# Optimization experiments

Hardware: AMD Instinct MI355X
Metric: run time of the kernel (lower is better)

## Reference

```python
import jax, jax.numpy as jnp
import numpy as np

BN_EPS = 1e-5
L2_EPS = 1e-12

def _conv2d(x, w, pad):
    # x: NCHW, w: OIHW
    return jax.lax.conv_general_dilated(
        x, w, window_strides=(1, 1), padding=[(pad, pad), (pad, pad)],
        dimension_numbers=('NCHW', 'OIHW', 'NCHW'))

def _l2norm(x, axis):
    n = jnp.sqrt(jnp.sum(x * x, axis=axis, keepdims=True))
    return x / jnp.maximum(n, L2_EPS)

def setup_inputs() -> dict:
    key = jax.random.key(0)
    ks = jax.random.split(key, 8)
    x = jax.random.normal(ks[0], (16, 512, 32, 32), dtype=jnp.float32)
    w_proj1 = jax.random.normal(ks[1], (512, 512, 3, 3), dtype=jnp.float32) * 0.02
    bn_gamma = jnp.ones((512,), dtype=jnp.float32)
    bn_beta = jnp.zeros((512,), dtype=jnp.float32)
    bn_mean = jnp.zeros((512,), dtype=jnp.float32)
    bn_var = jnp.ones((512,), dtype=jnp.float32)
    w_proj2 = jax.random.normal(ks[2], (512, 512, 3, 3), dtype=jnp.float32) * 0.02
    w_assign = jax.random.normal(ks[3], (64, 512, 1, 1), dtype=jnp.float32)
    centroids = jax.random.uniform(ks[4], (64, 512), dtype=jnp.float32)
    return {'x': x, 'w_proj1': w_proj1, 'bn_gamma': bn_gamma, 'bn_beta': bn_beta,
            'bn_mean': bn_mean, 'bn_var': bn_var, 'w_proj2': w_proj2,
            'w_assign': w_assign, 'centroids': centroids}

def reference(x, w_proj1, bn_gamma, bn_beta, bn_mean, bn_var, w_proj2, w_assign, centroids):
    # projection head: conv3x3 -> BN (eval) -> ReLU -> conv3x3
    h = _conv2d(x, w_proj1, pad=1)
    inv = jax.lax.rsqrt(bn_var + BN_EPS)
    h = (h - bn_mean[None, :, None, None]) * (bn_gamma * inv)[None, :, None, None] + bn_beta[None, :, None, None]
    h = jax.nn.relu(h)
    x_enc = _conv2d(h, w_proj2, pad=1)

    # descriptor-wise L2 normalization over channels
    xn = _l2norm(x_enc, axis=1)
    N, C, H, W = xn.shape
    K = w_assign.shape[0]

    # soft assignment: 1x1 conv -> softmax over clusters
    sa = _conv2d(xn, w_assign, pad=0).reshape(N, K, H * W)  # [N,K,L]
    sa = jax.nn.softmax(sa, axis=1)

    xf = xn.reshape(N, C, H * W)  # [N,C,L]
    # algebraic rewrite of the per-cluster residual loop:
    # vlad[n,k,c] = sum_l sa[n,k,l]*(xf[n,c,l] - cent[k,c])
    vlad = jnp.einsum('nkl,ncl->nkc', sa, xf) - sa.sum(-1)[:, :, None] * centroids[None]
    vlad = _l2norm(vlad, axis=2)          # intra-normalization
    vlad = vlad.reshape(N, K * C)
    vlad = _l2norm(vlad, axis=1)          # global L2 norm
    return (vlad, x_enc)
```

## Files before the change

### kernel.cpp

```cpp
#include <hip/hip_runtime.h>
#include <math.h>


typedef __bf16 bf16x8 __attribute__((ext_vector_type(8)));
typedef float f32x4 __attribute__((ext_vector_type(4)));

#define GLDS16(gp, lp)                                                  \
  __builtin_amdgcn_global_load_lds(                                     \
      (const __attribute__((address_space(1))) void*)(gp),              \
      (__attribute__((address_space(3))) void*)(lp), 16, 0, 0)

template <int MODE>
__global__ __launch_bounds__(256) void conv_gemm(
    const __bf16* __restrict__ in,
    const __bf16* __restrict__ wt,
    const float* __restrict__ scale, const float* __restrict__ shift,
    __bf16* __restrict__ outp) {
  __shared__ __align__(16) __bf16 Hl[6 * 42 * 64];
  __shared__ __align__(16) __bf16 Wl[2 * 128 * 64];

  const int t = threadIdx.x;
  const int bx = blockIdx.x, oT = blockIdx.y;
  const int lane = t & 63, wid = t >> 6;
  const int l16 = lane & 15, q = lane >> 4;
  const int wrow = wid >> 1, wcol = wid & 1;

  const int n = bx >> 3;
  const int trow0 = (bx & 7) * 4;

  const int swr = t >> 3, sp = t & 7;
  const __bf16* wsrc[4];
#pragma unroll
  for (int i = 0; i < 4; ++i)
    wsrc[i] = wt + (size_t)(oT * 128 + 32 * i + swr) * 4608 + sp * 8;

  const __bf16* inb = in + (size_t)n * (1156 * 512);
  const __bf16* hsrc[8];
  bool hval[8];
#pragma unroll
  for (int i = 0; i < 8; ++i) {
    const int jj = t + 256 * i;
    hval[i] = jj < 2016;
    const int hr = jj / 336;
    const int hrem = jj - hr * 336;
    const int hw = hrem >> 3, hc8 = hrem & 7;
    hsrc[i] = inb + ((size_t)((trow0 + hr) * 34 + hw)) * 512 +
              (hc8 ^ (hw & 7)) * 8;
  }

  const int c0 = (q ^ (l16 & 7)) * 8;
  const int c1 = ((4 + q) ^ (l16 & 7)) * 8;
  int aoff[4], prow_[4], pcol_[4];
#pragma unroll
  for (int i = 0; i < 4; ++i) {
    aoff[i] = (wrow * 64 + i * 16 + l16) * 64;
    const int p = wcol * 64 + i * 16 + l16;
    prow_[i] = p >> 5;
    pcol_[i] = p & 31;
  }

  f32x4 acc[4][4];
#pragma unroll
  for (int i = 0; i < 4; ++i)
#pragma unroll
    for (int j = 0; j < 4; ++j) acc[i][j] = (f32x4){0.f, 0.f, 0.f, 0.f};

#pragma unroll
  for (int i = 0; i < 8; ++i)
    if (hval[i]) GLDS16(hsrc[i], Hl + (t + 256 * i) * 8);
#pragma unroll
  for (int i = 0; i < 4; ++i)
    GLDS16(wsrc[i], Wl + (t + 256 * i) * 8);
#pragma unroll
  for (int i = 0; i < 4; ++i)
    GLDS16(wsrc[i] + 512, Wl + 8192 + (t + 256 * i) * 8);
  asm volatile("s_waitcnt vmcnt(4)" ::: "memory");
  __builtin_amdgcn_s_barrier();

  int tap = 0, dh = 0, dw = 0, cc = 0;
  int tap2 = 2, cc2 = 0;

#pragma unroll 1
  for (int s = 0; s < 72; ++s) {
    const int buf = (s & 1) << 13;
    const __bf16* Wb = Wl + buf;

    bf16x8 aw[4][2], bp[4][2];
#pragma unroll
    for (int i = 0; i < 4; ++i) {
      aw[i][0] = *(const bf16x8*)&Wb[aoff[i] + c0];
      aw[i][1] = *(const bf16x8*)&Wb[aoff[i] + c1];
    }
#pragma unroll
    for (int i = 0; i < 4; ++i) {
      const int col = pcol_[i] + dw;
      const int rb = (prow_[i] + dh) * 2688 + col * 64;
      const int xr = col & 7;
      bp[i][0] = *(const bf16x8*)&Hl[rb + (q ^ xr) * 8];
      bp[i][1] = *(const bf16x8*)&Hl[rb + ((4 + q) ^ xr) * 8];
    }
    asm volatile("s_waitcnt lgkmcnt(0)" ::: "memory");
    __builtin_amdgcn_sched_barrier(0);
    __builtin_amdgcn_s_barrier();

    if (tap == 8 && cc < 7) {
#pragma unroll
      for (int i = 0; i < 8; ++i)
        if (hval[i]) GLDS16(hsrc[i] + (cc + 1) * 64, Hl + (t + 256 * i) * 8);
    }
    if (s < 70) {
      const int woffs2 = (tap2 * 8 + cc2) * 64;
#pragma unroll
      for (int i = 0; i < 4; ++i)
        GLDS16(wsrc[i] + woffs2, Wl + buf + (t + 256 * i) * 8);
    }

    __builtin_amdgcn_s_setprio(1);
#pragma unroll
    for (int kh = 0; kh < 2; ++kh)
#pragma unroll
      for (int mt = 0; mt < 4; ++mt)
#pragma unroll
        for (int nt = 0; nt < 4; ++nt)
          acc[mt][nt] = __builtin_amdgcn_mfma_f32_16x16x32_bf16(
              aw[mt][kh], bp[nt][kh], acc[mt][nt], 0, 0, 0);
    __builtin_amdgcn_s_setprio(0);

    if (s < 70)
      asm volatile("s_waitcnt vmcnt(4)" ::: "memory");
    else
      asm volatile("s_waitcnt vmcnt(0)" ::: "memory");
    __builtin_amdgcn_s_barrier();

    ++tap;
    ++dw;
    if (dw == 3) {
      dw = 0;
      ++dh;
    }
    if (tap == 9) {
      tap = 0;
      dh = 0;
      dw = 0;
      ++cc;
    }
    if (++tap2 == 9) {
      tap2 = 0;
      ++cc2;
    }
  }

#pragma unroll
  for (int nt = 0; nt < 4; ++nt) {
    const int m_l = wcol * 64 + nt * 16 + l16;
    const int mg2 = bx * 128 + m_l;
    const int n2 = mg2 >> 10, pix2 = mg2 & 1023;
#pragma unroll
    for (int mt = 0; mt < 4; ++mt) {
      const int ob = oT * 128 + wrow * 64 + mt * 16 + q * 4;
      f32x4 v = acc[mt][nt];
      union {
        __bf16 b[4];
        uint2 u;
      } pk;
      if (MODE == 0) {
        const f32x4 sc = *(const f32x4*)&scale[ob];
        const f32x4 sh = *(const f32x4*)&shift[ob];
#pragma unroll
        for (int r = 0; r < 4; ++r)
          pk.b[r] = (__bf16)fmaxf(v[r] * sc[r] + sh[r], 0.f);
        __bf16* dst = outp +
                      ((size_t)n2 * 1156 + ((pix2 >> 5) + 1) * 34 +
                       ((pix2 & 31) + 1)) * 512 + ob;
        *(uint2*)dst = pk.u;
      } else {
#pragma unroll
        for (int r = 0; r < 4; ++r) pk.b[r] = (__bf16)v[r];
        __bf16* dst = outp + ((size_t)n2 * 1024 + pix2) * 512 + ob;
        *(uint2*)dst = pk.u;
      }
    }
  }
}

__global__ __launch_bounds__(256) void post_conv(
    const __bf16* __restrict__ xebT, const __bf16* __restrict__ watb,
    __bf16* __restrict__ saPb, float* __restrict__ S,
    float* __restrict__ xenc, __bf16* __restrict__ xeb) {
  __shared__ __align__(16) __bf16 Al[4][64 * 32];
  __shared__ __align__(16) __bf16 Wlb[4][64 * 32];
  __shared__ float Sl[64];
  const int t = threadIdx.x;
  const int bx0 = blockIdx.x;

  if (bx0 < 256) {
    const int pt = bx0 & 15, n = bx0 >> 4;
    const int lane = t & 63, wid = t >> 6;
    const int l16 = lane & 15, q = lane >> 4;
    if (t < 64) Sl[t] = 0.f;

    const int arow = t >> 2;
    const __bf16* asrc = xebT + ((size_t)n * 1024 + pt * 64 + arow) * 512 +
                         ((t & 3) ^ ((arow >> 1) & 3)) * 8;
    const __bf16* wsrc = watb + (size_t)(t >> 2) * 512 + (t & 3) * 8;
    const int ldsb = wid * 512;
    const int sw = (q ^ ((l16 >> 1) & 3)) * 8;
    const int pnoff = (t >> 2) * 32 + (t & 3) * 8;

    f32x4 acc[4];
#pragma unroll
    for (int i = 0; i < 4; ++i) acc[i] = (f32x4){0.f, 0.f, 0.f, 0.f};
    float pn = 0.f;

#pragma unroll
    for (int p = 0; p < 3; ++p) {
      GLDS16(asrc + p * 32, (__bf16*)Al[p] + ldsb);
      GLDS16(wsrc + p * 32, (__bf16*)Wlb[p] + ldsb);
    }
    asm volatile("s_waitcnt vmcnt(4)" ::: "memory");
    __builtin_amdgcn_s_barrier();

#pragma unroll 1
    for (int kc = 0; kc < 16; ++kc) {
      const __bf16* Ab = Al[kc & 3];
      const __bf16* Wb = Wlb[kc & 3];
      bf16x8 pv = *(const bf16x8*)&Ab[pnoff];
      bf16x8 pf = *(const bf16x8*)&Ab[(wid * 16 + l16) * 32 + sw];
      bf16x8 wf[4];
#pragma unroll
      for (int ka = 0; ka < 4; ++ka)
        wf[ka] = *(const bf16x8*)&Wb[(ka * 16 + l16) * 32 + sw];
      asm volatile("s_waitcnt lgkmcnt(0)" ::: "memory");
      __builtin_amdgcn_sched_barrier(0);
      __builtin_amdgcn_s_barrier();
      if (kc + 3 < 16) {
        GLDS16(asrc + (kc + 3) * 32, (__bf16*)Al[(kc + 3) & 3] + ldsb);
        GLDS16(wsrc + (kc + 3) * 32, (__bf16*)Wlb[(kc + 3) & 3] + ldsb);
      }
#pragma unroll
      for (int j = 0; j < 8; ++j) {
        float f = (float)pv[j];
        pn = fmaf(f, f, pn);
      }
#pragma unroll
      for (int ka = 0; ka < 4; ++ka)
        acc[ka] = __builtin_amdgcn_mfma_f32_16x16x32_bf16(wf[ka], pf, acc[ka],
                                                          0, 0, 0);
      if (kc < 13)
        asm volatile("s_waitcnt vmcnt(4)" ::: "memory");
      else
        asm volatile("s_waitcnt vmcnt(0)" ::: "memory");
      __builtin_amdgcn_s_barrier();
    }
    pn += __shfl_xor(pn, 1);
    pn += __shfl_xor(pn, 2);
    const float rn = 1.0f / fmaxf(sqrtf(__shfl(pn, l16 * 4)), 1e-12f);

    float sc[16];
    float m = -3.4e38f;
#pragma unroll
    for (int ka = 0; ka < 4; ++ka)
#pragma unroll
      for (int r = 0; r < 4; ++r) {
        float v = acc[ka][r] * rn;
        sc[ka * 4 + r] = v;
        m = fmaxf(m, v);
      }
    m = fmaxf(m, __shfl_xor(m, 16));
    m = fmaxf(m, __shfl_xor(m, 32));
    float s = 0.f;
#pragma unroll
    for (int j = 0; j < 16; ++j) {
      sc[j] = __expf(sc[j] - m);
      s += sc[j];
    }
    s += __shfl_xor(s, 16);
    s += __shfl_xor(s, 32);
    const float inv = 1.0f / s;
    const int pixg = pt * 64 + wid * 16 + l16;
#pragma unroll
    for (int j = 0; j < 16; ++j) {
      const int k = (j >> 2) * 16 + q * 4 + (j & 3);
      float sa = sc[j] * inv;
      sc[j] = sa;
      saPb[((size_t)n * 64 + k) * 1024 + pixg] = (__bf16)(sa * rn);
    }
#pragma unroll
    for (int j = 0; j < 16; ++j) {
      float v = sc[j];
      v += __shfl_xor(v, 1);
      v += __shfl_xor(v, 2);
      v += __shfl_xor(v, 4);
      v += __shfl_xor(v, 8);
      sc[j] = v;
    }
    if (l16 == 0) {
#pragma unroll
      for (int j = 0; j < 16; ++j)
        atomicAdd(&Sl[(j >> 2) * 16 + q * 4 + (j & 3)], sc[j]);
    }
    __syncthreads();
    if (t < 64) atomicAdd(&S[n * 64 + t], Sl[t]);
  } else {
    const int e = bx0 - 256;
    const int cc = e & 7, ptile = (e >> 3) & 15, n = e >> 7;
    __bf16* Ll = (__bf16*)Al;
    const int p0 = ptile * 64, c0 = cc * 64;
#pragma unroll
    for (int i = 0; i < 2; ++i) {
      const int u = t * 2 + i;
      const int pix = u >> 3, c8 = u & 7;
      uint4 v = *(const uint4*)&xebT[((size_t)n * 1024 + p0 + pix) * 512 + c0 +
                                     c8 * 8];
      *(uint4*)&Ll[pix * 64 + (c8 ^ (pix & 7)) * 8] = v;
    }
    __syncthreads();
    const int c = t >> 2, g = t & 3;
    union {
      float f[4];
      float4 v;
    } fv[4];
    union {
      __bf16 b[16];
      uint4 u[2];
    } bv;
#pragma unroll
    for (int r = 0; r < 16; ++r) {
      const int pix = g * 16 + r;
      __bf16 b = Ll[pix * 64 + ((c >> 3) ^ (pix & 7)) * 8 + (c & 7)];
      bv.b[r] = b;
      fv[r >> 2].f[r & 3] = (float)b;
    }
    float* fd = xenc + ((size_t)n * 512 + c0 + c) * 1024 + p0 + g * 16;
#pragma unroll
    for (int r = 0; r < 4; ++r) *(float4*)(fd + r * 4) = fv[r].v;
    __bf16* bd = xeb + ((size_t)n * 512 + c0 + c) * 1024 + p0 + g * 16;
    *(uint4*)bd = bv.u[0];
    *(uint4*)(bd + 8) = bv.u[1];
  }
}

__global__ __launch_bounds__(256) void vlad_gemm(
    const __bf16* __restrict__ saPb, const __bf16* __restrict__ xeb,
    float* __restrict__ vpart) {
  __shared__ __align__(16) __bf16 Al[4][64 * 32];
  __shared__ __align__(16) __bf16 Bl[4][128 * 32];

  const int t = threadIdx.x;
  const int cT = blockIdx.x, n = blockIdx.y, ks = blockIdx.z;
  const int lane = t & 63, wid = t >> 6;
  const int l16 = lane & 15, q = lane >> 4;
  const int wrow = wid >> 1, wcol = wid & 1;

  const int ar = t >> 2, acp = t & 3;
  const __bf16* asrc = saPb + (size_t)n * 65536 + (size_t)ar * 1024 + ks * 256 +
                       (acp ^ ((ar >> 1) & 3)) * 8;
  const int br0 = t >> 2, bcp0 = t & 3;
  const int br1 = (t + 256) >> 2, bcp1 = t & 3;
  const __bf16* bsrc0 = xeb + (size_t)n * 524288 +
                        (size_t)(cT * 128 + br0) * 1024 + ks * 256 +
                        (bcp0 ^ ((br0 >> 1) & 3)) * 8;
  const __bf16* bsrc1 = xeb + (size_t)n * 524288 +
                        (size_t)(cT * 128 + br1) * 1024 + ks * 256 +
                        (bcp1 ^ ((br1 >> 1) & 3)) * 8;

  const int ldsb = wid * 512;
  const int sw = (q ^ ((l16 >> 1) & 3)) * 8;

  f32x4 acc[2][4];
#pragma unroll
  for (int i = 0; i < 2; ++i)
#pragma unroll
    for (int j = 0; j < 4; ++j) acc[i][j] = (f32x4){0.f, 0.f, 0.f, 0.f};

#pragma unroll
  for (int p = 0; p < 3; ++p) {
    GLDS16(asrc + p * 32, (__bf16*)Al[p] + ldsb);
    GLDS16(bsrc0 + p * 32, (__bf16*)Bl[p] + ldsb);
    GLDS16(bsrc1 + p * 32, (__bf16*)Bl[p] + 2048 + ldsb);
  }
  asm volatile("s_waitcnt vmcnt(6)" ::: "memory");
  __builtin_amdgcn_s_barrier();

#pragma unroll 1
  for (int kc = 0; kc < 8; ++kc) {
    const __bf16* Ab = Al[kc & 3];
    const __bf16* Bb = Bl[kc & 3];
    bf16x8 af[2], bf[4];
#pragma unroll
    for (int i = 0; i < 2; ++i)
      af[i] = *(const bf16x8*)&Ab[(wrow * 32 + i * 16 + l16) * 32 + sw];
#pragma unroll
    for (int i = 0; i < 4; ++i)
      bf[i] = *(const bf16x8*)&Bb[(wcol * 64 + i * 16 + l16) * 32 + sw];
    asm volatile("s_waitcnt lgkmcnt(0)" ::: "memory");
    __builtin_amdgcn_sched_barrier(0);
    __builtin_amdgcn_s_barrier();
    if (kc + 3 < 8) {
      GLDS16(asrc + (kc + 3) * 32, (__bf16*)Al[(kc + 3) & 3] + ldsb);
      GLDS16(bsrc0 + (kc + 3) * 32, (__bf16*)Bl[(kc + 3) & 3] + ldsb);
      GLDS16(bsrc1 + (kc + 3) * 32, (__bf16*)Bl[(kc + 3) & 3] + 2048 + ldsb);
    }
#pragma unroll
    for (int mt = 0; mt < 2; ++mt)
#pragma unroll
      for (int nt = 0; nt < 4; ++nt)
        acc[mt][nt] = __builtin_amdgcn_mfma_f32_16x16x32_bf16(
            af[mt], bf[nt], acc[mt][nt], 0, 0, 0);
    if (kc < 5)
      asm volatile("s_waitcnt vmcnt(6)" ::: "memory");
    else
      asm volatile("s_waitcnt vmcnt(0)" ::: "memory");
    __builtin_amdgcn_s_barrier();
  }

  float* vp = vpart + (size_t)(ks * 16 + n) * 32768;
#pragma unroll
  for (int mt = 0; mt < 2; ++mt) {
    const int krow = wrow * 32 + mt * 16 + q * 4;
#pragma unroll
    for (int nt = 0; nt < 4; ++nt) {
      const int ccol = cT * 128 + wcol * 64 + nt * 16 + l16;
#pragma unroll
      for (int r = 0; r < 4; ++r)
        vp[(size_t)(krow + r) * 512 + ccol] = acc[mt][nt][r];
    }
  }
}

__global__ __launch_bounds__(64) void intra_norm(float* __restrict__ vraw,
                                                 const float* __restrict__ vpart,
                                                 const float* __restrict__ S,
                                                 const float* __restrict__ cent,
                                                 float* __restrict__ gss) {
  const int b = blockIdx.x;
  const int n = b >> 6, k = b & 63;
  const int lane = threadIdx.x;
  const float s = S[b];
  float v[8];
  float ss = 0.f;
#pragma unroll
  for (int j = 0; j < 8; ++j) {
    const int c = lane * 8 + j;
    const size_t off = (size_t)b * 512 + c;
    float val = vpart[off] + vpart[524288 + off] + vpart[2 * 524288 + off] +
                vpart[3 * 524288 + off] - s * cent[k * 512 + c];
    v[j] = val;
    ss += val * val;
  }
#pragma unroll
  for (int off = 1; off < 64; off <<= 1) ss += __shfl_xor(ss, off);
  const float rn = 1.0f / fmaxf(sqrtf(ss), 1e-12f);
#pragma unroll
  for (int j = 0; j < 8; ++j) vraw[(size_t)b * 512 + lane * 8 + j] = v[j] * rn;
  if (lane == 0) atomicAdd(&gss[n], ss * rn * rn);
}

__global__ __launch_bounds__(256) void finalize(const float* __restrict__ vraw,
                                                const float* __restrict__ gss,
                                                float* __restrict__ out) {
  const int base = blockIdx.x * 1024 + threadIdx.x;
#pragma unroll
  for (int j = 0; j < 4; ++j) {
    const int id = base + j * 256;
    const int n = id >> 15;
    out[id] = vraw[id] * (1.0f / fmaxf(sqrtf(gss[n]), 1e-12f));
  }
}

__global__ __launch_bounds__(256) void prep_all(
    const float* __restrict__ x, const float* __restrict__ w1,
    const float* __restrict__ w2, const float* __restrict__ g,
    const float* __restrict__ b, const float* __restrict__ m,
    const float* __restrict__ v, const float* __restrict__ wA,
    __bf16* __restrict__ xpad, __bf16* __restrict__ hpad,
    __bf16* __restrict__ wt1, __bf16* __restrict__ wt2,
    float* __restrict__ scale, float* __restrict__ shift,
    __bf16* __restrict__ watb, float* __restrict__ Sz) {
  __shared__ float Lw[4608];
  const int bx = blockIdx.x;
  const int t = threadIdx.x;

  if (bx < 1056) {
    const int which = bx >= 528;
    const int id = (which ? bx - 528 : bx) * 256 + t;
    const int n = id / 8448;
    const int rem = id - n * 8448;
    const int pb = rem >> 6;
    const int c8 = rem & 63;
    int h, w;
    if (pb < 34) {
      h = 0;
      w = pb;
    } else if (pb < 68) {
      h = 33;
      w = pb - 34;
    } else {
      const int r2 = pb - 68;
      h = 1 + (r2 >> 1);
      w = (r2 & 1) * 33;
    }
    __bf16* base = which ? hpad : xpad;
    *(uint4*)(base + ((size_t)n * 1156 + h * 34 + w) * 512 + c8 * 8) =
        (uint4){0u, 0u, 0u, 0u};
  } else if (bx < 1191) {
    const int i = (bx - 1056) * 256 + t;
    if (i < 512) {
      float sc = g[i] / sqrtf(v[i] + 1e-5f);
      scale[i] = sc;
      shift[i] = b[i] - m[i] * sc;
    } else if (i < 512 + 32768) {
      const int id = i - 512;
      const int k = id >> 9, j = id & 511;
      const int kt = j >> 5, cpos = (j >> 3) & 3, e = j & 7;
      const int c = kt * 32 + (cpos ^ ((k >> 1) & 3)) * 8 + e;
      watb[(size_t)k * 512 + j] = (__bf16)wA[(size_t)k * 512 + c];
    } else if (i < 512 + 32768 + 1040) {
      Sz[i - (512 + 32768)] = 0.f;
    }
  } else if (bx < 1703) {
    const int bb = bx - 1191;
    const int n = bb >> 5, h = bb & 31;
    const int w = t & 31, cg = t >> 5;
    const float* src = x + ((size_t)n * 512 + cg * 64) * 1024 + h * 32 + w;
    __bf16* dst =
        xpad + ((size_t)n * 1156 + (h + 1) * 34 + (w + 1)) * 512 + cg * 64;
    float fv[64];
#pragma unroll
    for (int j = 0; j < 64; ++j) fv[j] = src[j * 1024];
#pragma unroll
    for (int jj = 0; jj < 8; ++jj) {
      union {
        __bf16 b8[8];
        uint4 u;
      } pk;
#pragma unroll
      for (int j = 0; j < 8; ++j) pk.b8[j] = (__bf16)fv[jj * 8 + j];
      *(uint4*)(dst + jj * 8) = pk.u;
    }
  } else {
    const int bb = bx - 1703;
    const int o = bb & 511;
    const float* w = (bb >> 9) ? w2 : w1;
    __bf16* wt = (bb >> 9) ? wt2 : wt1;
#pragma unroll
    for (int i = 0; i < 18; ++i)
      Lw[t + 256 * i] = w[(size_t)o * 4608 + t + 256 * i];
    __syncthreads();
#pragma unroll
    for (int i = 0; i < 18; ++i) {
      const int idk = t + 256 * i;
      const int kt = idk >> 6;
      const int p = (idk >> 3) & 7, e = idk & 7;
      const int logical = p ^ (o & 7);
      const int k2 = kt * 64 + logical * 8 + e;
      const int tap = k2 >> 9, ci = k2 & 511;
      wt[(size_t)o * 4608 + idk] = (__bf16)Lw[ci * 9 + tap];
    }
  }
}

extern "C" void kernel_launch(void* const* d_in, const int* in_sizes, int n_in,
                              void* d_out, int out_size, void* d_ws,
                              size_t ws_size, hipStream_t stream) {
  const float* x = (const float*)d_in[0];
  const float* w1 = (const float*)d_in[1];
  const float* gam = (const float*)d_in[2];
  const float* bet = (const float*)d_in[3];
  const float* mean = (const float*)d_in[4];
  const float* var = (const float*)d_in[5];
  const float* w2 = (const float*)d_in[6];
  const float* wA = (const float*)d_in[7];
  const float* cent = (const float*)d_in[8];
  float* out = (float*)d_out;

  char* ws = (char*)d_ws;
  __bf16* Wt1 = (__bf16*)(ws + 0);
  __bf16* Wt2 = (__bf16*)(ws + 4718592);
  __bf16* xpad = (__bf16*)(ws + 9437184);
  __bf16* xebT = (__bf16*)(ws + 9437184);
  __bf16* saPb = (__bf16*)(ws + 26214400);
  __bf16* hpad = (__bf16*)(ws + 28377088);
  __bf16* xeb = (__bf16*)(ws + 28377088);
  float* vpart = (float*)(ws + 0);
  float* vraw = (float*)(ws + 8388608);
  float* scale = (float*)(ws + 47316992);
  float* shift = (float*)(ws + 47319040);
  __bf16* watb = (__bf16*)(ws + 47321088);
  float* S = (float*)(ws + 47386624);
  float* gss = (float*)(ws + 47390720);

  float* xenc = out + 524288;

  prep_all<<<2727, 256, 0, stream>>>(x, w1, w2, gam, bet, mean, var, wA, xpad,
                                     hpad, Wt1, Wt2, scale, shift, watb, S);

  conv_gemm<0><<<dim3(128, 4), 256, 0, stream>>>(xpad, Wt1, scale, shift, hpad);
  conv_gemm<1><<<dim3(128, 4), 256, 0, stream>>>(hpad, Wt2, nullptr, nullptr,
                                                 xebT);

  post_conv<<<2304, 256, 0, stream>>>(xebT, watb, saPb, S, xenc, xeb);
  vlad_gemm<<<dim3(4, 16, 4), 256, 0, stream>>>(saPb, xeb, vpart);
  intra_norm<<<1024, 64, 0, stream>>>(vraw, vpart, S, cent, gss);
  finalize<<<512, 256, 0, stream>>>(vraw, gss, out);
}
```

Baseline: 305.0 us.

## Merge post-conv, VLAD GEMM, intra-norm and finalize into one cooperative kernel

Replaces the four tail kernels with a single cooperative kernel of 512 persistent blocks that uses grid-wide syncs between phases. The transpose work is spread over a strided loop, and the GEMM, normalization and finalize stages reuse shared LDS. The goal is to remove three kernel launch gaps and the idle tail time between small kernels. In exchange it adds grid.sync overhead, needs all 512 blocks co-resident (launch bounds of 256 threads and 3 blocks per CU), and leaves fewer blocks for the transpose and finalize phases.

```diff
diff --git a/kernel.cpp b/kernel.cpp
--- a/kernel.cpp
+++ b/kernel.cpp
@@ -1,5 +1,8 @@
 #include <hip/hip_runtime.h>
+#include <hip/hip_cooperative_groups.h>
 #include <math.h>
+
+namespace cg = cooperative_groups;
 
 
 typedef __bf16 bf16x8 __attribute__((ext_vector_type(8)));
@@ -183,20 +186,25 @@
   }
 }
 
-__global__ __launch_bounds__(256) void post_conv(
+__global__ __launch_bounds__(256, 3) void tail_coop(
     const __bf16* __restrict__ xebT, const __bf16* __restrict__ watb,
     __bf16* __restrict__ saPb, float* __restrict__ S,
-    float* __restrict__ xenc, __bf16* __restrict__ xeb) {
-  __shared__ __align__(16) __bf16 Al[4][64 * 32];
-  __shared__ __align__(16) __bf16 Wlb[4][64 * 32];
-  __shared__ float Sl[64];
+    float* __restrict__ xenc, __bf16* __restrict__ xeb,
+    float* __restrict__ vpart, const float* __restrict__ cent,
+    float* __restrict__ vraw, float* __restrict__ gss,
+    float* __restrict__ out) {
+  __shared__ __align__(16) char SMEM[49152];
   const int t = threadIdx.x;
-  const int bx0 = blockIdx.x;
-
-  if (bx0 < 256) {
-    const int pt = bx0 & 15, n = bx0 >> 4;
-    const int lane = t & 63, wid = t >> 6;
-    const int l16 = lane & 15, q = lane >> 4;
+  const int bx = blockIdx.x;
+  const int lane = t & 63, wid = t >> 6;
+  const int l16 = lane & 15, q = lane >> 4;
+  cg::grid_group grid = cg::this_grid();
+
+  if (bx < 256) {
+    __bf16* Al = (__bf16*)SMEM;
+    __bf16* Wlb = (__bf16*)(SMEM + 16384);
+    float* Sl = (float*)(SMEM + 32768);
+    const int pt = bx & 15, n = bx >> 4;
     if (t < 64) Sl[t] = 0.f;
 
     const int arow = t >> 2;
@@ -214,16 +222,16 @@
 
 #pragma unroll
     for (int p = 0; p < 3; ++p) {
-      GLDS16(asrc + p * 32, (__bf16*)Al[p] + ldsb);
-      GLDS16(wsrc + p * 32, (__bf16*)Wlb[p] + ldsb);
+      GLDS16(asrc + p * 32, Al + p * 2048 + ldsb);
+      GLDS16(wsrc + p * 32, Wlb + p * 2048 + ldsb);
     }
     asm volatile("s_waitcnt vmcnt(4)" ::: "memory");
     __builtin_amdgcn_s_barrier();
 
 #pragma unroll 1
     for (int kc = 0; kc < 16; ++kc) {
-      const __bf16* Ab = Al[kc & 3];
-      const __bf16* Wb = Wlb[kc & 3];
+      const __bf16* Ab = Al + (kc & 3) * 2048;
+      const __bf16* Wb = Wlb + (kc & 3) * 2048;
       bf16x8 pv = *(const bf16x8*)&Ab[pnoff];
       bf16x8 pf = *(const bf16x8*)&Ab[(wid * 16 + l16) * 32 + sw];
       bf16x8 wf[4];
@@ -234,8 +242,8 @@
       __builtin_amdgcn_sched_barrier(0);
       __builtin_amdgcn_s_barrier();
       if (kc + 3 < 16) {
-        GLDS16(asrc + (kc + 3) * 32, (__bf16*)Al[(kc + 3) & 3] + ldsb);
-        GLDS16(wsrc + (kc + 3) * 32, (__bf16*)Wlb[(kc + 3) & 3] + ldsb);
+        GLDS16(asrc + (kc + 3) * 32, Al + ((kc + 3) & 3) * 2048 + ldsb);
+        GLDS16(wsrc + (kc + 3) * 32, Wlb + ((kc + 3) & 3) * 2048 + ldsb);
       }
 #pragma unroll
       for (int j = 0; j < 8; ++j) {
@@ -302,167 +310,167 @@
     __syncthreads();
     if (t < 64) atomicAdd(&S[n * 64 + t], Sl[t]);
   } else {
-    const int e = bx0 - 256;
-    const int cc = e & 7, ptile = (e >> 3) & 15, n = e >> 7;
-    __bf16* Ll = (__bf16*)Al;
-    const int p0 = ptile * 64, c0 = cc * 64;
-#pragma unroll
-    for (int i = 0; i < 2; ++i) {
-      const int u = t * 2 + i;
-      const int pix = u >> 3, c8 = u & 7;
-      uint4 v = *(const uint4*)&xebT[((size_t)n * 1024 + p0 + pix) * 512 + c0 +
-                                     c8 * 8];
-      *(uint4*)&Ll[pix * 64 + (c8 ^ (pix & 7)) * 8] = v;
-    }
-    __syncthreads();
-    const int c = t >> 2, g = t & 3;
-    union {
-      float f[4];
-      float4 v;
-    } fv[4];
-    union {
-      __bf16 b[16];
-      uint4 u[2];
-    } bv;
-#pragma unroll
-    for (int r = 0; r < 16; ++r) {
-      const int pix = g * 16 + r;
-      __bf16 b = Ll[pix * 64 + ((c >> 3) ^ (pix & 7)) * 8 + (c & 7)];
-      bv.b[r] = b;
-      fv[r >> 2].f[r & 3] = (float)b;
-    }
-    float* fd = xenc + ((size_t)n * 512 + c0 + c) * 1024 + p0 + g * 16;
-#pragma unroll
-    for (int r = 0; r < 4; ++r) *(float4*)(fd + r * 4) = fv[r].v;
-    __bf16* bd = xeb + ((size_t)n * 512 + c0 + c) * 1024 + p0 + g * 16;
-    *(uint4*)bd = bv.u[0];
-    *(uint4*)(bd + 8) = bv.u[1];
-  }
-}
-
-__global__ __launch_bounds__(256) void vlad_gemm(
-    const __bf16* __restrict__ saPb, const __bf16* __restrict__ xeb,
-    float* __restrict__ vpart) {
-  __shared__ __align__(16) __bf16 Al[4][64 * 32];
-  __shared__ __align__(16) __bf16 Bl[4][128 * 32];
-
-  const int t = threadIdx.x;
-  const int cT = blockIdx.x, n = blockIdx.y, ks = blockIdx.z;
-  const int lane = t & 63, wid = t >> 6;
-  const int l16 = lane & 15, q = lane >> 4;
-  const int wrow = wid >> 1, wcol = wid & 1;
-
-  const int ar = t >> 2, acp = t & 3;
-  const __bf16* asrc = saPb + (size_t)n * 65536 + (size_t)ar * 1024 + ks * 256 +
-                       (acp ^ ((ar >> 1) & 3)) * 8;
-  const int br0 = t >> 2, bcp0 = t & 3;
-  const int br1 = (t + 256) >> 2, bcp1 = t & 3;
-  const __bf16* bsrc0 = xeb + (size_t)n * 524288 +
-                        (size_t)(cT * 128 + br0) * 1024 + ks * 256 +
-                        (bcp0 ^ ((br0 >> 1) & 3)) * 8;
-  const __bf16* bsrc1 = xeb + (size_t)n * 524288 +
-                        (size_t)(cT * 128 + br1) * 1024 + ks * 256 +
-                        (bcp1 ^ ((br1 >> 1) & 3)) * 8;
-
-  const int ldsb = wid * 512;
-  const int sw = (q ^ ((l16 >> 1) & 3)) * 8;
-
-  f32x4 acc[2][4];
-#pragma unroll
-  for (int i = 0; i < 2; ++i)
-#pragma unroll
-    for (int j = 0; j < 4; ++j) acc[i][j] = (f32x4){0.f, 0.f, 0.f, 0.f};
-
-#pragma unroll
-  for (int p = 0; p < 3; ++p) {
-    GLDS16(asrc + p * 32, (__bf16*)Al[p] + ldsb);
-    GLDS16(bsrc0 + p * 32, (__bf16*)Bl[p] + ldsb);
-    GLDS16(bsrc1 + p * 32, (__bf16*)Bl[p] + 2048 + ldsb);
-  }
-  asm volatile("s_waitcnt vmcnt(6)" ::: "memory");
-  __builtin_amdgcn_s_barrier();
-
+    __bf16* Ll = (__bf16*)SMEM;
 #pragma unroll 1
-  for (int kc = 0; kc < 8; ++kc) {
-    const __bf16* Ab = Al[kc & 3];
-    const __bf16* Bb = Bl[kc & 3];
-    bf16x8 af[2], bf[4];
+    for (int e = bx - 256; e < 2048; e += 256) {
+      const int cc = e & 7, ptile = (e >> 3) & 15, n = e >> 7;
+      const int p0 = ptile * 64, c0 = cc * 64;
+#pragma unroll
+      for (int i = 0; i < 2; ++i) {
+        const int u = t * 2 + i;
+        const int pix = u >> 3, c8 = u & 7;
+        uint4 v = *(const uint4*)&xebT[((size_t)n * 1024 + p0 + pix) * 512 +
+                                       c0 + c8 * 8];
+        *(uint4*)&Ll[pix * 64 + (c8 ^ (pix & 7)) * 8] = v;
+      }
+      __syncthreads();
+      const int c = t >> 2, g = t & 3;
+      union {
+        float f[4];
+        float4 v;
+      } fv[4];
+      union {
+        __bf16 b[16];
+        uint4 u[2];
+      } bv;
+#pragma unroll
+      for (int r = 0; r < 16; ++r) {
+        const int pix = g * 16 + r;
+        __bf16 b = Ll[pix * 64 + ((c >> 3) ^ (pix & 7)) * 8 + (c & 7)];
+        bv.b[r] = b;
+        fv[r >> 2].f[r & 3] = (float)b;
+      }
+      float* fd = xenc + ((size_t)n * 512 + c0 + c) * 1024 + p0 + g * 16;
+#pragma unroll
+      for (int r = 0; r < 4; ++r) *(float4*)(fd + r * 4) = fv[r].v;
+      __bf16* bd = xeb + ((size_t)n * 512 + c0 + c) * 1024 + p0 + g * 16;
+      *(uint4*)bd = bv.u[0];
+      *(uint4*)(bd + 8) = bv.u[1];
+      __syncthreads();
+    }
+  }
+
+  __threadfence();
+  grid.sync();
+
+  if (bx < 256) {
+    __bf16* Av = (__bf16*)SMEM;
+    __bf16* Bv = (__bf16*)(SMEM + 16384);
+    const int cT = bx & 3, n = (bx >> 2) & 15, ks = bx >> 6;
+    const int wrow = wid >> 1, wcol = wid & 1;
+
+    const int ar = t >> 2, acp = t & 3;
+    const __bf16* asrc = saPb + (size_t)n * 65536 + (size_t)ar * 1024 +
+                         ks * 256 + (acp ^ ((ar >> 1) & 3)) * 8;
+    const int br0 = t >> 2, bcp0 = t & 3;
+    const int br1 = (t + 256) >> 2, bcp1 = t & 3;
+    const __bf16* bsrc0 = xeb + (size_t)n * 524288 +
+                          (size_t)(cT * 128 + br0) * 1024 + ks * 256 +
+                          (bcp0 ^ ((br0 >> 1) & 3)) * 8;
+    const __bf16* bsrc1 = xeb + (size_t)n * 524288 +
+                          (size_t)(cT * 128 + br1) * 1024 + ks * 256 +
+                          (bcp1 ^ ((br1 >> 1) & 3)) * 8;
+
+    const int ldsb = wid * 512;
+    const int sw = (q ^ ((l16 >> 1) & 3)) * 8;
+
+    f32x4 acc[2][4];
 #pragma unroll
     for (int i = 0; i < 2; ++i)
-      af[i] = *(const bf16x8*)&Ab[(wrow * 32 + i * 16 + l16) * 32 + sw];
-#pragma unroll
-    for (int i = 0; i < 4; ++i)
-      bf[i] = *(const bf16x8*)&Bb[(wcol * 64 + i * 16 + l16) * 32 + sw];
-    asm volatile("s_waitcnt lgkmcnt(0)" ::: "memory");
-    __builtin_amdgcn_sched_barrier(0);
+#pragma unroll
+      for (int j = 0; j < 4; ++j) acc[i][j] = (f32x4){0.f, 0.f, 0.f, 0.f};
+
+#pragma unroll
+    for (int p = 0; p < 3; ++p) {
+      GLDS16(asrc + p * 32, Av + p * 2048 + ldsb);
+      GLDS16(bsrc0 + p * 32, Bv + p * 4096 + ldsb);
+      GLDS16(bsrc1 + p * 32, Bv + p * 4096 + 2048 + ldsb);
+    }
+    asm volatile("s_waitcnt vmcnt(6)" ::: "memory");
     __builtin_amdgcn_s_barrier();
-    if (kc + 3 < 8) {
-      GLDS16(asrc + (kc + 3) * 32, (__bf16*)Al[(kc + 3) & 3] + ldsb);
-      GLDS16(bsrc0 + (kc + 3) * 32, (__bf16*)Bl[(kc + 3) & 3] + ldsb);
-      GLDS16(bsrc1 + (kc + 3) * 32, (__bf16*)Bl[(kc + 3) & 3] + 2048 + ldsb);
-    }
-#pragma unroll
-    for (int mt = 0; mt < 2; ++mt)
-#pragma unroll
-      for (int nt = 0; nt < 4; ++nt)
-        acc[mt][nt] = __builtin_amdgcn_mfma_f32_16x16x32_bf16(
-            af[mt], bf[nt], acc[mt][nt], 0, 0, 0);
-    if (kc < 5)
-      asm volatile("s_waitcnt vmcnt(6)" ::: "memory");
-    else
-      asm volatile("s_waitcnt vmcnt(0)" ::: "memory");
-    __builtin_amdgcn_s_barrier();
-  }
-
-  float* vp = vpart + (size_t)(ks * 16 + n) * 32768;
-#pragma unroll
-  for (int mt = 0; mt < 2; ++mt) {
-    const int krow = wrow * 32 + mt * 16 + q * 4;
-#pragma unroll
-    for (int nt = 0; nt < 4; ++nt) {
-      const int ccol = cT * 128 + wcol * 64 + nt * 16 + l16;
-#pragma unroll
-      for (int r = 0; r < 4; ++r)
-        vp[(size_t)(krow + r) * 512 + ccol] = acc[mt][nt][r];
-    }
-  }
-}
-
-__global__ __launch_bounds__(64) void intra_norm(float* __restrict__ vraw,
-                                                 const float* __restrict__ vpart,
-                                                 const float* __restrict__ S,
-                                                 const float* __restrict__ cent,
-                                                 float* __restrict__ gss) {
-  const int b = blockIdx.x;
-  const int n = b >> 6, k = b & 63;
-  const int lane = threadIdx.x;
-  const float s = S[b];
-  float v[8];
-  float ss = 0.f;
-#pragma unroll
-  for (int j = 0; j < 8; ++j) {
-    const int c = lane * 8 + j;
-    const size_t off = (size_t)b * 512 + c;
-    float val = vpart[off] + vpart[524288 + off] + vpart[2 * 524288 + off] +
-                vpart[3 * 524288 + off] - s * cent[k * 512 + c];
-    v[j] = val;
-    ss += val * val;
-  }
-#pragma unroll
-  for (int off = 1; off < 64; off <<= 1) ss += __shfl_xor(ss, off);
-  const float rn = 1.0f / fmaxf(sqrtf(ss), 1e-12f);
-#pragma unroll
-  for (int j = 0; j < 8; ++j) vraw[(size_t)b * 512 + lane * 8 + j] = v[j] * rn;
-  if (lane == 0) atomicAdd(&gss[n], ss * rn * rn);
-}
-
-__global__ __launch_bounds__(256) void finalize(const float* __restrict__ vraw,
-                                                const float* __restrict__ gss,
-                                                float* __restrict__ out) {
-  const int base = blockIdx.x * 1024 + threadIdx.x;
-#pragma unroll
-  for (int j = 0; j < 4; ++j) {
-    const int id = base + j * 256;
+
+#pragma unroll 1
+    for (int kc = 0; kc < 8; ++kc) {
+      const __bf16* Ab = Av + (kc & 3) * 2048;
+      const __bf16* Bb = Bv + (kc & 3) * 4096;
+      bf16x8 af[2], bf[4];
+#pragma unroll
+      for (int i = 0; i < 2; ++i)
+        af[i] = *(const bf16x8*)&Ab[(wrow * 32 + i * 16 + l16) * 32 + sw];
+#pragma unroll
+      for (int i = 0; i < 4; ++i)
+        bf[i] = *(const bf16x8*)&Bb[(wcol * 64 + i * 16 + l16) * 32 + sw];
+      asm volatile("s_waitcnt lgkmcnt(0)" ::: "memory");
+      __builtin_amdgcn_sched_barrier(0);
+      __builtin_amdgcn_s_barrier();
+      if (kc + 3 < 8) {
+        GLDS16(asrc + (kc + 3) * 32, Av + ((kc + 3) & 3) * 2048 + ldsb);
+        GLDS16(bsrc0 + (kc + 3) * 32, Bv + ((kc + 3) & 3) * 4096 + ldsb);
+        GLDS16(bsrc1 + (kc + 3) * 32,
+               Bv + ((kc + 3) & 3) * 4096 + 2048 + ldsb);
+      }
+#pragma unroll
+      for (int mt = 0; mt < 2; ++mt)
+#pragma unroll
+        for (int nt = 0; nt < 4; ++nt)
+          acc[mt][nt] = __builtin_amdgcn_mfma_f32_16x16x32_bf16(
+              af[mt], bf[nt], acc[mt][nt], 0, 0, 0);
+      if (kc < 5)
+        asm volatile("s_waitcnt vmcnt(6)" ::: "memory");
+      else
+        asm volatile("s_waitcnt vmcnt(0)" ::: "memory");
+      __builtin_amdgcn_s_barrier();
+    }
+
+    float* vp = vpart + (size_t)(ks * 16 + n) * 32768;
+#pragma unroll
+    for (int mt = 0; mt < 2; ++mt) {
+      const int krow = wrow * 32 + mt * 16 + q * 4;
+#pragma unroll
+      for (int nt = 0; nt < 4; ++nt) {
+        const int ccol = cT * 128 + wcol * 64 + nt * 16 + l16;
+#pragma unroll
+        for (int r = 0; r < 4; ++r)
+          vp[(size_t)(krow + r) * 512 + ccol] = acc[mt][nt][r];
+      }
+    }
+  }
+
+  __threadfence();
+  grid.sync();
+
+  {
+    const int b = bx * 4 + wid;
+    if (b < 1024) {
+      const int n = b >> 6, k = b & 63;
+      const float s = S[b];
+      float v[8];
+      float ss = 0.f;
+#pragma unroll
+      for (int j = 0; j < 8; ++j) {
+        const int c = lane * 8 + j;
+        const size_t off = (size_t)b * 512 + c;
+        float val = vpart[off] + vpart[524288 + off] +
+                    vpart[2 * 524288 + off] + vpart[3 * 524288 + off] -
+                    s * cent[k * 512 + c];
+        v[j] = val;
+        ss += val * val;
+      }
+#pragma unroll
+      for (int off = 1; off < 64; off <<= 1) ss += __shfl_xor(ss, off);
+      const float rn = 1.0f / fmaxf(sqrtf(ss), 1e-12f);
+#pragma unroll
+      for (int j = 0; j < 8; ++j)
+        vraw[(size_t)b * 512 + lane * 8 + j] = v[j] * rn;
+      if (lane == 0) atomicAdd(&gss[n], ss * rn * rn);
+    }
+  }
+
+  __threadfence();
+  grid.sync();
+
+#pragma unroll 1
+  for (int id = bx * 256 + t; id < 524288; id += 512 * 256) {
     const int n = id >> 15;
     out[id] = vraw[id] * (1.0f / fmaxf(sqrtf(gss[n]), 1e-12f));
   }
@@ -599,8 +607,8 @@
   conv_gemm<1><<<dim3(128, 4), 256, 0, stream>>>(hpad, Wt2, nullptr, nullptr,
                                                  xebT);
 
-  post_conv<<<2304, 256, 0, stream>>>(xebT, watb, saPb, S, xenc, xeb);
-  vlad_gemm<<<dim3(4, 16, 4), 256, 0, stream>>>(saPb, xeb, vpart);
-  intra_norm<<<1024, 64, 0, stream>>>(vraw, vpart, S, cent, gss);
-  finalize<<<512, 256, 0, stream>>>(vraw, gss, out);
+  void* args[] = {&xebT, &watb, &saPb, &S,    &xenc, &xeb,
+                  &vpart, &cent, &vraw, &gss, &out};
+  hipLaunchCooperativeKernel((void*)tail_coop, dim3(512), dim3(256), args, 0,
+                             stream);
 }
```

After: 662.9 us. 117% more time.
